# Kernel optimization log

Measured on AMD Instinct MI355X. Metric: run time of the kernel, lower is better.

The kernel has to match this reference:

```python
import jax, jax.numpy as jnp
import numpy as np

N_NODES = 100000
N_EDGES = 3200000


def setup_inputs() -> dict:
    key = jax.random.key(0)
    ks = jax.random.split(key, 8)
    x = jax.random.normal(ks[0], (N_NODES, 8), dtype=jnp.float32)
    edge_index = jax.random.randint(ks[1], (2, N_EDGES), 0, N_NODES, dtype=jnp.int64)
    # glorot-style scaled params (ARMAConv init_weight, root_weight, bias per stack/layer)
    def g(k, fi, fo):
        return jax.random.normal(k, (fi, fo), dtype=jnp.float32) * np.float32(1.0 / np.sqrt(fi))
    W1 = g(ks[2], 8, 16)   # conv1 init_weight
    V1 = g(ks[3], 8, 16)   # conv1 root_weight
    b1 = jnp.zeros((16,), jnp.float32)
    W2 = g(ks[4], 16, 16)  # conv2 init_weight
    V2 = g(ks[5], 16, 16)  # conv2 root_weight
    b2 = jnp.zeros((16,), jnp.float32)
    return {"x": x, "edge_index": edge_index, "W1": W1, "V1": V1, "b1": b1,
            "W2": W2, "V2": V2, "b2": b2}


def reference(x, edge_index, W1, V1, b1, W2, V2, b2):
    n = x.shape[0]
    row, col = edge_index[0], edge_index[1]  # source -> target
    # gcn_norm without self loops: norm_e = deg(col)^-1/2 * deg(row)^-1/2 ... PyG uses deg over col
    ones = jnp.ones(row.shape[0], dtype=x.dtype)
    deg = jax.ops.segment_sum(ones, col, num_segments=n)
    dinv = jnp.where(deg > 0, jax.lax.rsqrt(jnp.maximum(deg, 1e-30)), 0.0).astype(x.dtype)
    norm = dinv[row] * dinv[col]  # [E]

    def arma_conv(h, W, V, b):
        # T=1, K=1 ARMA: relu(A_norm @ (h W) + h V + b)
        m = (h @ W)[row] * norm[:, None]            # gather + edge scale [E, F]
        agg = jax.ops.segment_sum(m, col, num_segments=n)  # scatter-add to targets
        return jax.nn.relu(agg + h @ V + b)

    # Note: ARMAConv applies act=ReLU internally; outer .relu() after conv1 is idempotent.
    h = arma_conv(x, W1, V1, b1)
    return arma_conv(h, W2, V2, b2)
```

## Files before the change

### kernel.cpp

```cpp
#include <hip/hip_runtime.h>


#define WC 128
#define LG2WC 7
#define MAXB 1024
#define NBC 256
#define SCAP 8192

typedef unsigned uintv4 __attribute__((ext_vector_type(4)));

__device__ inline unsigned bf16rte(float x) {
    unsigned u = __float_as_uint(x);
    return (u + 0x7FFFu + ((u >> 16) & 1u)) >> 16;
}

__global__ __launch_bounds__(1024)
void chunk_sort(const int* __restrict__ row, const int* __restrict__ col,
                int* __restrict__ srt, int* __restrict__ histg,
                int* __restrict__ segst, int E, int B, int chunkE) {
    __shared__ int hist[MAXB];
    __shared__ int cur[MAXB];
    __shared__ int tsum[MAXB];
    int i = blockIdx.x, t = threadIdx.x;
    hist[t] = 0;
    __syncthreads();
    int lo = i * chunkE, hi = lo + chunkE; if (hi > E) hi = E;
    for (int e = lo + t; e < hi; e += 1024)
        atomicAdd(&hist[col[e] >> LG2WC], 1);
    __syncthreads();
    int v = hist[t];
    tsum[t] = v;
    __syncthreads();
    for (int off = 1; off < 1024; off <<= 1) {
        int u = 0;
        if (t >= off) u = tsum[t - off];
        __syncthreads();
        if (t >= off) tsum[t] += u;
        __syncthreads();
    }
    cur[t] = tsum[t] - v;
    __syncthreads();
    if (t < B) {
        histg[(size_t)i * B + t] = hist[t];
        segst[(size_t)i * B + t] = cur[t];
    }
    __syncthreads();
    for (int e = lo + t; e < hi; e += 1024) {
        int c = col[e];
        int r = row[e];
        int pos = lo + atomicAdd(&cur[c >> LG2WC], 1);
        srt[pos] = ((c & (WC - 1)) << 17) | r;
    }
}

__global__ void tot8_kernel(const int* __restrict__ histg, int* __restrict__ part, int B) {
    int idx = blockIdx.x * blockDim.x + threadIdx.x;
    if (idx >= 8 * B) return;
    int k = idx / B, j = idx - k * B;
    int s = 0;
    for (int i = k * 32; i < k * 32 + 32; i++) s += histg[(size_t)i * B + j];
    part[(size_t)k * B + j] = s;
}

__global__ void scan1024_kernel(const int* __restrict__ part, int* __restrict__ base, int B) {
    __shared__ int s[1024];
    int t = threadIdx.x;
    int v = 0;
    if (t < B) {
#pragma unroll
        for (int k = 0; k < 8; k++) v += part[(size_t)k * B + t];
    }
    s[t] = v;
    __syncthreads();
    for (int off = 1; off < 1024; off <<= 1) {
        int u = 0;
        if (t >= off) u = s[t - off];
        __syncthreads();
        if (t >= off) s[t] += u;
        __syncthreads();
    }
    if (t < B) base[t] = s[t] - v;
}

__global__ void bucket_sort(const int* __restrict__ srt, const int* __restrict__ histg,
                            const int* __restrict__ segst, const int* __restrict__ bbase,
                            int* __restrict__ ptr, int* __restrict__ srt2,
                            float* __restrict__ dinv, int E, int n, int B, int chunkE) {
    __shared__ int hrow[NBC];
    __shared__ int srow[NBC];
    __shared__ int spref[NBC];
    __shared__ int stage[SCAP];
    __shared__ int tsum[256];
    __shared__ int cnt[WC], colb[WC], ccur[WC];
    __shared__ int Ssh;
    int j = blockIdx.x, t = threadIdx.x;
    hrow[t] = histg[(size_t)t * B + j];
    srow[t] = segst[(size_t)t * B + j];
    if (t < WC) cnt[t] = 0;
    __syncthreads();
    int v = hrow[t];
    tsum[t] = v;
    __syncthreads();
    for (int off = 1; off < 256; off <<= 1) {
        int u = 0;
        if (t >= off) u = tsum[t - off];
        __syncthreads();
        if (t >= off) tsum[t] += u;
        __syncthreads();
    }
    spref[t] = tsum[t] - v;
    if (t == 255) Ssh = tsum[255];
    __syncthreads();
    int S = Ssh;
    int gbase = bbase[j];
    bool fits = (S <= SCAP);
    if (fits) {
        int src = t * chunkE + srow[t];
        int dst = spref[t];
        int len = hrow[t];
        for (int q = 0; q < len; q++) stage[dst + q] = srt[src + q];
        __syncthreads();
        for (int e = t; e < S; e += 256) atomicAdd(&cnt[stage[e] >> 17], 1);
    } else {
        int src = t * chunkE + srow[t];
        int len = hrow[t];
        for (int q = 0; q < len; q++) atomicAdd(&cnt[srt[src + q] >> 17], 1);
    }
    __syncthreads();
    if (t < WC) colb[t] = cnt[t];
    __syncthreads();
    for (int off = 1; off < WC; off <<= 1) {
        int u = 0;
        if (t >= off && t < WC) u = colb[t - off];
        __syncthreads();
        if (t >= off && t < WC) colb[t] += u;
        __syncthreads();
    }
    if (t < WC) {
        int excl = colb[t] - cnt[t];
        int c = j * WC + t;
        ccur[t] = gbase + excl;
        if (c < n) {
            ptr[c] = gbase + excl;
            dinv[c] = cnt[t] > 0 ? rsqrtf((float)cnt[t]) : 0.0f;
        }
    }
    if (j == B - 1 && t == 0) ptr[n] = E;
    __syncthreads();
    if (fits) {
        for (int e = t; e < S; e += 256) {
            int pk = stage[e];
            int pos = atomicAdd(&ccur[pk >> 17], 1);
            srt2[pos] = pk & 0x1FFFF;
        }
    } else {
        int src = t * chunkE + srow[t];
        int len = hrow[t];
        for (int q = 0; q < len; q++) {
            int pk = srt[src + q];
            int pos = atomicAdd(&ccur[pk >> 17], 1);
            srt2[pos] = pk & 0x1FFFF;
        }
    }
}

template <int FI>
__global__ void proj_kernel(const float* __restrict__ hin, const float* __restrict__ W,
                            const float* __restrict__ dinv, unsigned* __restrict__ p, int n) {
    __shared__ float sW[FI * 16];
    for (int t = threadIdx.x; t < FI * 16; t += blockDim.x) sW[t] = W[t];
    __syncthreads();
    int i = blockIdx.x * blockDim.x + threadIdx.x;
    if (i >= n) return;
    float hi[FI];
    const float4* hr = (const float4*)(hin + (size_t)i * FI);
#pragma unroll
    for (int k = 0; k < FI / 4; k++) {
        float4 v = hr[k];
        hi[4 * k] = v.x; hi[4 * k + 1] = v.y; hi[4 * k + 2] = v.z; hi[4 * k + 3] = v.w;
    }
    float di = dinv[i];
    float outv[16];
#pragma unroll
    for (int f = 0; f < 16; f++) {
        float s = 0.0f;
#pragma unroll
        for (int k = 0; k < FI; k++) s += hi[k] * sW[k * 16 + f];
        outv[f] = s * di;
    }
    uint4 u0, u1;
    u0.x = bf16rte(outv[0])  | (bf16rte(outv[1])  << 16);
    u0.y = bf16rte(outv[2])  | (bf16rte(outv[3])  << 16);
    u0.z = bf16rte(outv[4])  | (bf16rte(outv[5])  << 16);
    u0.w = bf16rte(outv[6])  | (bf16rte(outv[7])  << 16);
    u1.x = bf16rte(outv[8])  | (bf16rte(outv[9])  << 16);
    u1.y = bf16rte(outv[10]) | (bf16rte(outv[11]) << 16);
    u1.z = bf16rte(outv[12]) | (bf16rte(outv[13]) << 16);
    u1.w = bf16rte(outv[14]) | (bf16rte(outv[15]) << 16);
    uint4* pr = (uint4*)(p + (size_t)i * 8);
    pr[0] = u0;
    pr[1] = u1;
}

template <int FI>
__global__ __launch_bounds__(256, 4)
void gather_finish_kernel(const int* __restrict__ ptr, const int* __restrict__ srt2,
                          const uintv4* __restrict__ p, const float* hin,
                          const float* __restrict__ V, const float* __restrict__ b,
                          const float* __restrict__ dinv, float* out, int n) {
    __shared__ float sV[FI * 16];
    __shared__ float sb[16];
    for (int t = threadIdx.x; t < FI * 16; t += blockDim.x) sV[t] = V[t];
    if (threadIdx.x < 16) sb[threadIdx.x] = b[threadIdx.x];
    __syncthreads();
    int g = blockIdx.x * (blockDim.x >> 2) + (threadIdx.x >> 2);
    int hb = threadIdx.x & 1;
    int sh = (threadIdx.x >> 1) & 1;
    if (g >= n) return;
    int s0 = ptr[g], s1 = ptr[g + 1];
    int mid = (s0 + s1) >> 1;
    int e0 = sh ? mid : s0;
    int e1 = sh ? s1 : mid;
    const uintv4* pb = p + hb;
    float a0 = 0, a1 = 0, a2 = 0, a3 = 0, a4 = 0, a5 = 0, a6 = 0, a7 = 0;
    for (int e = e0; e < e1; e += 8) {
        int r[8];
#pragma unroll
        for (int q = 0; q < 8; q++) {
            int idx = e + q;
            r[q] = __builtin_nontemporal_load(srt2 + (idx < e1 ? idx : e1 - 1));
        }
        uintv4 u[8];
#pragma unroll
        for (int q = 0; q < 8; q++) u[q] = pb[(size_t)r[q] * 2];
#pragma unroll
        for (int q = 0; q < 8; q++) {
            if (e + q >= e1) u[q] = (uintv4)0;
            a0 += __uint_as_float(u[q][0] << 16);
            a1 += __uint_as_float(u[q][0] & 0xFFFF0000u);
            a2 += __uint_as_float(u[q][1] << 16);
            a3 += __uint_as_float(u[q][1] & 0xFFFF0000u);
            a4 += __uint_as_float(u[q][2] << 16);
            a5 += __uint_as_float(u[q][2] & 0xFFFF0000u);
            a6 += __uint_as_float(u[q][3] << 16);
            a7 += __uint_as_float(u[q][3] & 0xFFFF0000u);
        }
    }
    a0 += __shfl_xor(a0, 2);
    a1 += __shfl_xor(a1, 2);
    a2 += __shfl_xor(a2, 2);
    a3 += __shfl_xor(a3, 2);
    a4 += __shfl_xor(a4, 2);
    a5 += __shfl_xor(a5, 2);
    a6 += __shfl_xor(a6, 2);
    a7 += __shfl_xor(a7, 2);
    if (sh != 0) return;
    int f0 = hb * 8;
    float hi[FI];
    const float4* h4 = (const float4*)(hin + (size_t)g * FI);
#pragma unroll
    for (int k = 0; k < FI / 4; k++) {
        float4 v = h4[k];
        hi[4 * k] = v.x; hi[4 * k + 1] = v.y; hi[4 * k + 2] = v.z; hi[4 * k + 3] = v.w;
    }
    float hv[8] = {0, 0, 0, 0, 0, 0, 0, 0};
#pragma unroll
    for (int k = 0; k < FI; k++) {
        float hk = hi[k];
#pragma unroll
        for (int q = 0; q < 8; q++) hv[q] += hk * sV[k * 16 + f0 + q];
    }
    float di = dinv[g];
    float rr[8] = {a0, a1, a2, a3, a4, a5, a6, a7};
#pragma unroll
    for (int q = 0; q < 8; q++) {
        float r_ = sb[f0 + q] + di * rr[q] + hv[q];
        rr[q] = r_ > 0.0f ? r_ : 0.0f;
    }
    float4* o4 = (float4*)(out + (size_t)g * 16 + f0);
    o4[0] = make_float4(rr[0], rr[1], rr[2], rr[3]);
    o4[1] = make_float4(rr[4], rr[5], rr[6], rr[7]);
}

extern "C" void kernel_launch(void* const* d_in, const int* in_sizes, int n_in,
                              void* d_out, int out_size, void* d_ws, size_t ws_size,
                              hipStream_t stream) {
    const float* x  = (const float*)d_in[0];
    const int*   ei = (const int*)d_in[1];
    const float* W1 = (const float*)d_in[2];
    const float* V1 = (const float*)d_in[3];
    const float* b1 = (const float*)d_in[4];
    const float* W2 = (const float*)d_in[5];
    const float* V2 = (const float*)d_in[6];
    const float* b2 = (const float*)d_in[7];

    const int n = in_sizes[0] / 8;
    const int E = in_sizes[1] / 2;
    const int* row = ei;
    const int* col = ei + E;

    const int B = (n + WC - 1) / WC;
    const int chunkE = (E + NBC - 1) / NBC;

    auto align = [](size_t v) { return (v + 255) / 256 * 256; };
    char* ws = (char*)d_ws;
    size_t off = 0;
    float* dinv  = (float*)(ws + off); off += align((size_t)n * 4);
    int*   ptr   = (int*)(ws + off);   off += align((size_t)(n + 1) * 4);
    int*   histg = (int*)(ws + off);   off += align((size_t)NBC * B * 4);
    int*   segst = (int*)(ws + off);   off += align((size_t)NBC * B * 4);
    int*   part  = (int*)(ws + off);   off += align((size_t)8 * B * 4);
    int*   bbase = (int*)(ws + off);   off += align((size_t)B * 4);
    int*      srt = (int*)(ws + off);
    unsigned* p   = (unsigned*)(ws + off); off += align((size_t)E * 4);
    int*      srt2 = (int*)(ws + off);     off += align((size_t)E * 4);
    float* out = (float*)d_out;

    const int bs = 256;
    const int gbN = (n + bs - 1) / bs;
    const int gbG = (n * 4 + bs - 1) / bs;

    chunk_sort<<<NBC, 1024, 0, stream>>>(row, col, srt, histg, segst, E, B, chunkE);
    tot8_kernel<<<(8 * B + bs - 1) / bs, bs, 0, stream>>>(histg, part, B);
    scan1024_kernel<<<1, 1024, 0, stream>>>(part, bbase, B);
    bucket_sort<<<B, bs, 0, stream>>>(srt, histg, segst, bbase, ptr, srt2, dinv, E, n, B, chunkE);

    proj_kernel<8><<<gbN, bs, 0, stream>>>(x, W1, dinv, p, n);
    gather_finish_kernel<8><<<gbG, bs, 0, stream>>>(ptr, srt2, (const uintv4*)p, x, V1, b1, dinv, out, n);

    proj_kernel<16><<<gbN, bs, 0, stream>>>(out, W2, dinv, p, n);
    gather_finish_kernel<16><<<gbG, bs, 0, stream>>>(ptr, srt2, (const uintv4*)p, out, V2, b2, dinv, out, n);
}
```

Before: 150.1 us.

## Cache sort ranks in registers and degree-sort nodes for gather balance

chunk_sort now reads col/row once, keeps the packed edge and its atomic rank in registers, and scatters with the scanned offsets. This removes the second pass over the edge arrays. bucket_sort likewise reuses the ranks from its counting atomics instead of doing a second round of atomics. Three new kernels build a degree histogram, scan it and scatter node ids into a degree-ordered permutation. The gather kernels use that permutation so that neighbouring wavefronts get similar edge counts. In exchange there are extra launches and an indirection that breaks locality of node-indexed reads and writes.

```diff
diff --git a/kernel.cpp b/kernel.cpp
--- a/kernel.cpp
+++ b/kernel.cpp
@@ -6,6 +6,8 @@
 #define MAXB 1024
 #define NBC 256
 #define SCAP 8192
+#define CITER 13
+#define SITER 32
 
 typedef unsigned uintv4 __attribute__((ext_vector_type(4)));
 
@@ -25,8 +27,22 @@
     hist[t] = 0;
     __syncthreads();
     int lo = i * chunkE, hi = lo + chunkE; if (hi > E) hi = E;
-    for (int e = lo + t; e < hi; e += 1024)
-        atomicAdd(&hist[col[e] >> LG2WC], 1);
+    int pk_[CITER];
+    unsigned br_[CITER];
+#pragma unroll
+    for (int q = 0; q < CITER; q++) {
+        int e = lo + t + q * 1024;
+        int pkv = 0; unsigned brv = 0xFFFFFFFFu;
+        if (e < hi) {
+            int c = col[e];
+            int r = row[e];
+            int bkt = c >> LG2WC;
+            int rank = atomicAdd(&hist[bkt], 1);
+            pkv = ((c & (WC - 1)) << 17) | r;
+            brv = (unsigned)bkt | ((unsigned)rank << 10);
+        }
+        pk_[q] = pkv; br_[q] = brv;
+    }
     __syncthreads();
     int v = hist[t];
     tsum[t] = v;
@@ -44,12 +60,13 @@
         histg[(size_t)i * B + t] = hist[t];
         segst[(size_t)i * B + t] = cur[t];
     }
-    __syncthreads();
-    for (int e = lo + t; e < hi; e += 1024) {
-        int c = col[e];
-        int r = row[e];
-        int pos = lo + atomicAdd(&cur[c >> LG2WC], 1);
-        srt[pos] = ((c & (WC - 1)) << 17) | r;
+#pragma unroll
+    for (int q = 0; q < CITER; q++) {
+        if (br_[q] != 0xFFFFFFFFu) {
+            int bkt = br_[q] & 1023;
+            int rank = (int)(br_[q] >> 10);
+            srt[lo + cur[bkt] + rank] = pk_[q];
+        }
     }
 }
 
@@ -91,7 +108,7 @@
     __shared__ int spref[NBC];
     __shared__ int stage[SCAP];
     __shared__ int tsum[256];
-    __shared__ int cnt[WC], colb[WC], ccur[WC];
+    __shared__ int cnt[WC], colb[WC], cexc[WC];
     __shared__ int Ssh;
     int j = blockIdx.x, t = threadIdx.x;
     hrow[t] = histg[(size_t)t * B + j];
@@ -114,13 +131,20 @@
     int S = Ssh;
     int gbase = bbase[j];
     bool fits = (S <= SCAP);
+    int rk_[SITER];
     if (fits) {
         int src = t * chunkE + srow[t];
         int dst = spref[t];
         int len = hrow[t];
         for (int q = 0; q < len; q++) stage[dst + q] = srt[src + q];
         __syncthreads();
-        for (int e = t; e < S; e += 256) atomicAdd(&cnt[stage[e] >> 17], 1);
+#pragma unroll
+        for (int q = 0; q < SITER; q++) {
+            int e = t + q * 256;
+            int rv = -1;
+            if (e < S) rv = atomicAdd(&cnt[stage[e] >> 17], 1);
+            rk_[q] = rv;
+        }
     } else {
         int src = t * chunkE + srow[t];
         int len = hrow[t];
@@ -139,7 +163,7 @@
     if (t < WC) {
         int excl = colb[t] - cnt[t];
         int c = j * WC + t;
-        ccur[t] = gbase + excl;
+        cexc[t] = gbase + excl;
         if (c < n) {
             ptr[c] = gbase + excl;
             dinv[c] = cnt[t] > 0 ? rsqrtf((float)cnt[t]) : 0.0f;
@@ -148,19 +172,81 @@
     if (j == B - 1 && t == 0) ptr[n] = E;
     __syncthreads();
     if (fits) {
-        for (int e = t; e < S; e += 256) {
-            int pk = stage[e];
-            int pos = atomicAdd(&ccur[pk >> 17], 1);
-            srt2[pos] = pk & 0x1FFFF;
+#pragma unroll
+        for (int q = 0; q < SITER; q++) {
+            int e = t + q * 256;
+            if (e < S) {
+                int pk = stage[e];
+                srt2[cexc[pk >> 17] + rk_[q]] = pk & 0x1FFFF;
+            }
         }
     } else {
         int src = t * chunkE + srow[t];
         int len = hrow[t];
         for (int q = 0; q < len; q++) {
             int pk = srt[src + q];
-            int pos = atomicAdd(&ccur[pk >> 17], 1);
+            int pos = atomicAdd(&cexc[pk >> 17], 1);
             srt2[pos] = pk & 0x1FFFF;
         }
+    }
+}
+
+__global__ __launch_bounds__(1024)
+void deg_hist_kernel(const int* __restrict__ ptr, int* __restrict__ dhist, int n) {
+    __shared__ int h[256];
+    int blk = blockIdx.x, t = threadIdx.x;
+    if (t < 256) h[t] = 0;
+    __syncthreads();
+    int i = blk * 1024 + t;
+    if (i < n) {
+        int d = ptr[i + 1] - ptr[i];
+        atomicAdd(&h[d < 255 ? d : 255], 1);
+    }
+    __syncthreads();
+    if (t < 256) dhist[(size_t)blk * 256 + t] = h[t];
+}
+
+__global__ __launch_bounds__(1024)
+void deg_scan_kernel(const int* __restrict__ dhist, int* __restrict__ dbase, int nb2) {
+    __shared__ int s[1024];
+    int t = threadIdx.x;
+    int M = 256 * nb2;
+    int chunk = (M + 1023) / 1024;
+    int lo = t * chunk, hi = lo + chunk; if (hi > M) hi = M;
+    int sum = 0;
+    for (int m = lo; m < hi; m++) {
+        int bin = m / nb2, blk = m - bin * nb2;
+        sum += dhist[(size_t)blk * 256 + bin];
+    }
+    s[t] = sum;
+    __syncthreads();
+    for (int off = 1; off < 1024; off <<= 1) {
+        int u = 0;
+        if (t >= off) u = s[t - off];
+        __syncthreads();
+        if (t >= off) s[t] += u;
+        __syncthreads();
+    }
+    int run = s[t] - sum;
+    for (int m = lo; m < hi; m++) {
+        int bin = m / nb2, blk = m - bin * nb2;
+        dbase[(size_t)blk * 256 + bin] = run;
+        run += dhist[(size_t)blk * 256 + bin];
+    }
+}
+
+__global__ __launch_bounds__(1024)
+void deg_scatter_kernel(const int* __restrict__ ptr, const int* __restrict__ dbase,
+                        int* __restrict__ perm, int n) {
+    __shared__ int cur[256];
+    int blk = blockIdx.x, t = threadIdx.x;
+    if (t < 256) cur[t] = dbase[(size_t)blk * 256 + t];
+    __syncthreads();
+    int i = blk * 1024 + t;
+    if (i < n) {
+        int d = ptr[i + 1] - ptr[i];
+        int pos = atomicAdd(&cur[d < 255 ? d : 255], 1);
+        perm[pos] = i;
     }
 }
 
@@ -207,16 +293,18 @@
 void gather_finish_kernel(const int* __restrict__ ptr, const int* __restrict__ srt2,
                           const uintv4* __restrict__ p, const float* hin,
                           const float* __restrict__ V, const float* __restrict__ b,
-                          const float* __restrict__ dinv, float* out, int n) {
+                          const float* __restrict__ dinv, const int* __restrict__ perm,
+                          float* out, int n) {
     __shared__ float sV[FI * 16];
     __shared__ float sb[16];
     for (int t = threadIdx.x; t < FI * 16; t += blockDim.x) sV[t] = V[t];
     if (threadIdx.x < 16) sb[threadIdx.x] = b[threadIdx.x];
     __syncthreads();
-    int g = blockIdx.x * (blockDim.x >> 2) + (threadIdx.x >> 2);
+    int gg = blockIdx.x * (blockDim.x >> 2) + (threadIdx.x >> 2);
     int hb = threadIdx.x & 1;
     int sh = (threadIdx.x >> 1) & 1;
-    if (g >= n) return;
+    if (gg >= n) return;
+    int g = perm[gg];
     int s0 = ptr[g], s1 = ptr[g + 1];
     int mid = (s0 + s1) >> 1;
     int e0 = sh ? mid : s0;
@@ -301,6 +389,7 @@
 
     const int B = (n + WC - 1) / WC;
     const int chunkE = (E + NBC - 1) / NBC;
+    const int nb2 = (n + 1023) / 1024;
 
     auto align = [](size_t v) { return (v + 255) / 256 * 256; };
     char* ws = (char*)d_ws;
@@ -311,6 +400,9 @@
     int*   segst = (int*)(ws + off);   off += align((size_t)NBC * B * 4);
     int*   part  = (int*)(ws + off);   off += align((size_t)8 * B * 4);
     int*   bbase = (int*)(ws + off);   off += align((size_t)B * 4);
+    int*   dhist = (int*)(ws + off);   off += align((size_t)nb2 * 256 * 4);
+    int*   dbase = (int*)(ws + off);   off += align((size_t)nb2 * 256 * 4);
+    int*   perm  = (int*)(ws + off);   off += align((size_t)n * 4);
     int*      srt = (int*)(ws + off);
     unsigned* p   = (unsigned*)(ws + off); off += align((size_t)E * 4);
     int*      srt2 = (int*)(ws + off);     off += align((size_t)E * 4);
@@ -325,9 +417,13 @@
     scan1024_kernel<<<1, 1024, 0, stream>>>(part, bbase, B);
     bucket_sort<<<B, bs, 0, stream>>>(srt, histg, segst, bbase, ptr, srt2, dinv, E, n, B, chunkE);
 
+    deg_hist_kernel<<<nb2, 1024, 0, stream>>>(ptr, dhist, n);
+    deg_scan_kernel<<<1, 1024, 0, stream>>>(dhist, dbase, nb2);
+    deg_scatter_kernel<<<nb2, 1024, 0, stream>>>(ptr, dbase, perm, n);
+
     proj_kernel<8><<<gbN, bs, 0, stream>>>(x, W1, dinv, p, n);
-    gather_finish_kernel<8><<<gbG, bs, 0, stream>>>(ptr, srt2, (const uintv4*)p, x, V1, b1, dinv, out, n);
+    gather_finish_kernel<8><<<gbG, bs, 0, stream>>>(ptr, srt2, (const uintv4*)p, x, V1, b1, dinv, perm, out, n);
 
     proj_kernel<16><<<gbN, bs, 0, stream>>>(out, W2, dinv, p, n);
-    gather_finish_kernel<16><<<gbG, bs, 0, stream>>>(ptr, srt2, (const uintv4*)p, out, V2, b2, dinv, out, n);
-}
+    gather_finish_kernel<16><<<gbG, bs, 0, stream>>>(ptr, srt2, (const uintv4*)p, out, V2, b2, dinv, perm, out, n);
+}
```

Measured after the change: 226.6 us. 1.51x slower.
